# Kernel tuning notes

Measured on AMD Instinct MI355X. Metric: run time of the kernel, lower is better.

The kernel has to match this reference:

```python
import jax, jax.numpy as jnp
import numpy as np

LEVELS = 5          # perfect binary tree depth
N_NODES = 2**LEVELS - 1  # 31, level-order: children of p are 2p+1, 2p+2
V, E, ENC, H, LBL = 50000, 128, 128, 128, 104
B, L = 64, 128


def setup_inputs() -> dict:
    key = jax.random.key(0)
    ks = jax.random.split(key, 16)
    g = lambda k, shape: (jax.random.normal(k, shape, dtype=jnp.float32) * 0.02)
    return {
        "tokens": jax.random.randint(ks[0], (B, L, N_NODES), 0, V),
        "embedding": g(ks[1], (V, E)),
        "Wc_w": g(ks[2], (ENC, E)),
        "Wc_b": g(ks[3], (ENC,)),
        "Wih_f": g(ks[4], (3 * H, ENC)),
        "Whh_f": g(ks[5], (3 * H, H)),
        "bih_f": g(ks[6], (3 * H,)),
        "bhh_f": g(ks[7], (3 * H,)),
        "Wih_b": g(ks[8], (3 * H, ENC)),
        "Whh_b": g(ks[9], (3 * H, H)),
        "bih_b": g(ks[10], (3 * H,)),
        "bhh_b": g(ks[11], (3 * H,)),
        "Wout": g(ks[12], (LBL, 2 * H)),
        "bout": g(ks[13], (LBL,)),
    }


def _tree_encode(tokens, embedding, Wc_w, Wc_b):
    # node encoding h(n) = W_c(emb(tok_n)) + sum(children h); statement enc = max over nodes
    x = embedding[tokens]                       # [B, L, N, E] gather
    h = jnp.einsum("blne,ce->blnc", x, Wc_w) + Wc_b  # [B, L, N, ENC]
    for lvl in reversed(range(LEVELS - 1)):     # bottom-up accumulation
        s = 2**lvl - 1
        n = 2**lvl
        cs = 2 * s + 1                          # first child index of this level
        left = h[..., cs:cs + 2 * n:2, :]
        right = h[..., cs + 1:cs + 2 * n:2, :]
        h = h.at[..., s:s + n, :].add(left + right)
    # node_list max across all recursion calls == max over all tree nodes
    return jnp.max(h, axis=2)                   # [B, L, ENC]


def _gru_dir(xs, Wih, Whh, bih, bhh, reverse):
    # xs: [B, L, ENC]; PyTorch GRU cell equations, h0 = 0
    gi = jnp.einsum("blc,gc->blg", xs, Wih) + bih  # precompute input gates [B, L, 3H]
    h0 = jnp.zeros((xs.shape[0], H), dtype=xs.dtype)

    def step(h, gi_t):
        gh = h @ Whh.T + bhh
        ir, iz, inn = jnp.split(gi_t, 3, axis=-1)
        hr, hz, hn = jnp.split(gh, 3, axis=-1)
        r = jax.nn.sigmoid(ir + hr)
        z = jax.nn.sigmoid(iz + hz)
        n = jnp.tanh(inn + r * hn)
        h_new = (1.0 - z) * n + z * h
        return h_new, h_new

    _, ys = jax.lax.scan(step, h0, gi.transpose(1, 0, 2), reverse=reverse)
    return ys.transpose(1, 0, 2)                # [B, L, H]


def reference(tokens, embedding, Wc_w, Wc_b,
              Wih_f, Whh_f, bih_f, bhh_f,
              Wih_b, Whh_b, bih_b, bhh_b,
              Wout, bout):
    encodes = _tree_encode(tokens, embedding, Wc_w, Wc_b)   # [B, L, ENC]
    fwd = _gru_dir(encodes, Wih_f, Whh_f, bih_f, bhh_f, reverse=False)
    bwd = _gru_dir(encodes, Wih_b, Whh_b, bih_b, bhh_b, reverse=True)
    gru_out = jnp.concatenate([fwd, bwd], axis=-1)          # [B, L, 2H]
    pooled = jnp.max(gru_out, axis=1)                       # max_pool1d over time
    return pooled @ Wout.T + bout                           # [B, LBL]
```

## Files before the change

### kernel.cpp

```cpp
#include <hip/hip_runtime.h>
#include <hip/hip_bf16.h>
#include <math.h>

#define NN   31
#define VV   50000
#define EE   128
#define HH   128
#define BB   64
#define LL   128
#define NLBL 104

template <bool BIAS>
__global__ __launch_bounds__(256, 2) void gemm128(const float* __restrict__ A,
                                                  const float* __restrict__ B0,
                                                  const float* __restrict__ B1,
                                                  const float* __restrict__ bias0,
                                                  const float* __restrict__ bias1,
                                                  float* __restrict__ C0,
                                                  float* __restrict__ C1,
                                                  int M, int N) {
    const float* Bm  = blockIdx.z ? B1 : B0;
    const float* bias = blockIdx.z ? bias1 : bias0;
    float* C = blockIdx.z ? C1 : C0;

    __shared__ float4 As[64 * 17];
    __shared__ float4 Bs[128 * 17];
    const int tid = threadIdx.x;
    const int m0 = blockIdx.x * 64;
    const int n0 = blockIdx.y * 128;
    const float4* Af4 = (const float4*)A;
    const float4* Bf4 = (const float4*)Bm;

    const int r0 = (tid >> 4) * 4;
    const int cb = tid & 15;
    float acc[4][8] = {};

    for (int kk = 0; kk < 2; ++kk) {
        for (int f = tid; f < 128 * 16; f += 256) {
            int r = f >> 4, e = f & 15;
            Bs[r * 17 + e] = Bf4[(size_t)(n0 + r) * 32 + kk * 16 + e];
        }
        for (int f = tid; f < 64 * 16; f += 256) {
            int r = f >> 4, e = f & 15;
            float4 v = make_float4(0.f, 0.f, 0.f, 0.f);
            if (m0 + r < M) v = Af4[(size_t)(m0 + r) * 32 + kk * 16 + e];
            As[r * 17 + e] = v;
        }
        __syncthreads();
        #pragma unroll
        for (int e = 0; e < 16; ++e) {
            float4 a[4], b[8];
            #pragma unroll
            for (int i = 0; i < 4; ++i) a[i] = As[(r0 + i) * 17 + e];
            #pragma unroll
            for (int j = 0; j < 8; ++j) b[j] = Bs[(cb + j * 16) * 17 + e];
            #pragma unroll
            for (int i = 0; i < 4; ++i) {
                #pragma unroll
                for (int j = 0; j < 8; ++j) {
                    acc[i][j] += a[i].x * b[j].x;
                    acc[i][j] += a[i].y * b[j].y;
                    acc[i][j] += a[i].z * b[j].z;
                    acc[i][j] += a[i].w * b[j].w;
                }
            }
        }
        __syncthreads();
    }

    #pragma unroll
    for (int i = 0; i < 4; ++i) {
        int row = m0 + r0 + i;
        if (row < M) {
            #pragma unroll
            for (int j = 0; j < 8; ++j) {
                int col = n0 + cb + j * 16;
                float v = acc[i][j];
                if (BIAS) v += bias[col];
                C[(size_t)row * N + col] = v;
            }
        }
    }
}

__global__ __launch_bounds__(256) void tree_encode(const int* __restrict__ tok,
                                                   const float* __restrict__ Wemb,
                                                   const float* __restrict__ Wcb,
                                                   float* __restrict__ enc) {
    __shared__ int st[2][NN];
    const int tid = threadIdx.x;
    const int p = tid >> 7;
    const int c = tid & 127;
    const int bl = blockIdx.x * 2;
    if (tid < 2 * NN) {
        int pp = tid / NN, jj = tid - pp * NN;
        st[pp][jj] = tok[(size_t)(bl + pp) * NN + jj];
    }
    __syncthreads();

    float v[NN];
    #pragma unroll
    for (int j = 0; j < NN; ++j)
        v[j] = Wemb[(size_t)st[p][j] * 128 + c];
    #pragma unroll
    for (int i = 14; i >= 0; --i)
        v[i] += v[2 * i + 1] + v[2 * i + 2];

    const float wb = Wcb[c];
    float m = v[0] + 31.f * wb;
    #pragma unroll
    for (int i = 1; i <= 2; ++i)  m = fmaxf(m, v[i] + 15.f * wb);
    #pragma unroll
    for (int i = 3; i <= 6; ++i)  m = fmaxf(m, v[i] + 7.f * wb);
    #pragma unroll
    for (int i = 7; i <= 14; ++i) m = fmaxf(m, v[i] + 3.f * wb);
    #pragma unroll
    for (int i = 15; i <= 30; ++i) m = fmaxf(m, v[i] + wb);

    enc[(size_t)(bl + p) * 128 + c] = m;
}

__device__ __forceinline__ float sigm(float x) { return 1.f / (1.f + __expf(-x)); }
__device__ __forceinline__ float tanh_f(float x) { return 1.f - 2.f / (1.f + __expf(2.f * x)); }

__device__ __forceinline__ float dpp_xor1(float x) {
    return __builtin_bit_cast(float,
        __builtin_amdgcn_mov_dpp(__builtin_bit_cast(int, x), 0xB1, 0xF, 0xF, true));
}
__device__ __forceinline__ float dpp_xor2(float x) {
    return __builtin_bit_cast(float,
        __builtin_amdgcn_mov_dpp(__builtin_bit_cast(int, x), 0x4E, 0xF, 0xF, true));
}
__device__ __forceinline__ float quad_sum(float x) {
    x += dpp_xor1(x);
    x += dpp_xor2(x);
    return x;
}

__global__ __launch_bounds__(256, 1) void gru_scan(const float* __restrict__ gi_f,
                                                   const float* __restrict__ gi_b,
                                                   const float* __restrict__ Whh_f,
                                                   const float* __restrict__ Whh_b,
                                                   const float* __restrict__ bhh_f,
                                                   const float* __restrict__ bhh_b,
                                                   float* __restrict__ pooled) {
    const int tid = threadIdx.x;
    const int g   = tid >> 2;
    const int p   = tid & 3;
    const int dir = blockIdx.x & 1;
    const int b   = blockIdx.x >> 1;
    const float* gi  = dir ? gi_b  : gi_f;
    const float* Whh = dir ? Whh_b : Whh_f;
    const float* bhh = dir ? bhh_b : bhh_f;

    __shared__ __align__(16) float hbuf[2][128];

    float4 w[6][8];
    const float4* wf4 = (const float4*)Whh;
    #pragma unroll
    for (int r6 = 0; r6 < 6; ++r6)
        #pragma unroll
        for (int q = 0; q < 8; ++q)
            w[r6][q] = wf4[(size_t)(r6 * 64 + g) * 32 + p * 8 + q];

    const int c = g + p * 64;
    float bh_r = 0.f, bh_z = 0.f, bh_n = 0.f;
    if (p < 2) { bh_r = bhh[c]; bh_z = bhh[128 + c]; bh_n = bhh[256 + c]; }

    float hold = 0.f, m = -INFINITY;
    if (tid < 128) { hbuf[0][tid] = 0.f; }

    float gr = 0.f, gz = 0.f, gn = 0.f;
    {
        const int t0 = dir ? (LL - 1) : 0;
        const float* grow = gi + ((size_t)b * LL + t0) * 384;
        if (p < 2) { gr = grow[c]; gz = grow[128 + c]; gn = grow[256 + c]; }
    }
    __syncthreads();

    for (int s = 0; s < LL; ++s) {
        const int cur = s & 1;
        float gr_n = 0.f, gz_n = 0.f, gn_n = 0.f;
        if (p < 2 && s + 1 < LL) {
            const int t1 = dir ? (LL - 2 - s) : (s + 1);
            const float* grow = gi + ((size_t)b * LL + t1) * 384;
            gr_n = grow[c]; gz_n = grow[128 + c]; gn_n = grow[256 + c];
        }

        const float4* hq = ((const float4*)hbuf[cur]) + p * 8;
        float a0 = 0.f, a1 = 0.f, a2 = 0.f, a3 = 0.f, a4 = 0.f, a5 = 0.f;
        #pragma unroll
        for (int q = 0; q < 8; ++q) {
            const float4 hv = hq[q];
            a0 += w[0][q].x * hv.x + w[0][q].y * hv.y + w[0][q].z * hv.z + w[0][q].w * hv.w;
            a1 += w[1][q].x * hv.x + w[1][q].y * hv.y + w[1][q].z * hv.z + w[1][q].w * hv.w;
            a2 += w[2][q].x * hv.x + w[2][q].y * hv.y + w[2][q].z * hv.z + w[2][q].w * hv.w;
            a3 += w[3][q].x * hv.x + w[3][q].y * hv.y + w[3][q].z * hv.z + w[3][q].w * hv.w;
            a4 += w[4][q].x * hv.x + w[4][q].y * hv.y + w[4][q].z * hv.z + w[4][q].w * hv.w;
            a5 += w[5][q].x * hv.x + w[5][q].y * hv.y + w[5][q].z * hv.z + w[5][q].w * hv.w;
        }
        a0 = quad_sum(a0); a1 = quad_sum(a1); a2 = quad_sum(a2);
        a3 = quad_sum(a3); a4 = quad_sum(a4); a5 = quad_sum(a5);

        if (p < 2) {
            const float ghr = (p ? a1 : a0) + bh_r;
            const float ghz = (p ? a3 : a2) + bh_z;
            const float ghn = (p ? a5 : a4) + bh_n;
            const float r = sigm(gr + ghr);
            const float z = sigm(gz + ghz);
            const float n = tanh_f(gn + r * ghn);
            const float hn = (1.f - z) * n + z * hold;
            hold = hn;
            m = fmaxf(m, hn);
            hbuf[cur ^ 1][c] = hn;
        }
        gr = gr_n; gz = gz_n; gn = gn_n;
        __syncthreads();
    }
    if (p < 2) pooled[((size_t)b * 2 + dir) * 128 + c] = m;
}

__global__ __launch_bounds__(128) void out_head(const float* __restrict__ pooled,
                                                const float* __restrict__ Wout,
                                                const float* __restrict__ bout,
                                                float* __restrict__ out) {
    __shared__ __align__(16) float pbuf[256];
    const int b = blockIdx.x, o = threadIdx.x;
    if (o < 64) ((float4*)pbuf)[o] = ((const float4*)(pooled + (size_t)b * 256))[o];
    __syncthreads();
    if (o < NLBL) {
        float acc = bout[o];
        const float4* wf4 = (const float4*)(Wout + (size_t)o * 256);
        const float4* pf4 = (const float4*)pbuf;
        #pragma unroll 8
        for (int q = 0; q < 64; ++q) {
            float4 wv = wf4[q], pv = pf4[q];
            acc += wv.x * pv.x + wv.y * pv.y + wv.z * pv.z + wv.w * pv.w;
        }
        out[(size_t)b * NLBL + o] = acc;
    }
}

extern "C" void kernel_launch(void* const* d_in, const int* in_sizes, int n_in,
                              void* d_out, int out_size, void* d_ws, size_t ws_size,
                              hipStream_t stream) {
    const int*   tokens = (const int*)  d_in[0];
    const float* emb    = (const float*)d_in[1];
    const float* Wc_w   = (const float*)d_in[2];
    const float* Wc_b   = (const float*)d_in[3];
    const float* Wih_f  = (const float*)d_in[4];
    const float* Whh_f  = (const float*)d_in[5];
    const float* bih_f  = (const float*)d_in[6];
    const float* bhh_f  = (const float*)d_in[7];
    const float* Wih_b  = (const float*)d_in[8];
    const float* Whh_b  = (const float*)d_in[9];
    const float* bih_b  = (const float*)d_in[10];
    const float* bhh_b  = (const float*)d_in[11];
    const float* Wout   = (const float*)d_in[12];
    const float* bout   = (const float*)d_in[13];
    float* out = (float*)d_out;
    float* ws  = (float*)d_ws;

    float* Wemb = ws;
    float* enc  = Wemb + (size_t)VV * 128;
    float* gi_f = enc  + (size_t)BB * LL * 128;
    float* gi_b = gi_f + (size_t)BB * LL * 384;
    float* pool = gi_b + (size_t)BB * LL * 384;

    gemm128<false><<<dim3(782, 1, 1), 256, 0, stream>>>(
        emb, Wc_w, Wc_w, nullptr, nullptr, Wemb, Wemb, VV, 128);
    tree_encode<<<dim3(4096), 256, 0, stream>>>(tokens, Wemb, Wc_b, enc);
    gemm128<true><<<dim3(128, 3, 2), 256, 0, stream>>>(
        enc, Wih_f, Wih_b, bih_f, bih_b, gi_f, gi_b, BB * LL, 384);
    gru_scan<<<dim3(128), 256, 0, stream>>>(gi_f, gi_b, Whh_f, Whh_b, bhh_f, bhh_b, pool);
    out_head<<<dim3(64), 128, 0, stream>>>(pool, Wout, bout, out);
}
```

Before: 295.2 us.

## Widen GRU scan to 512 threads with one hidden unit per quad

The recurrent scan block grows from 256 to 512 threads. Each quad of four lanes now owns a single hidden unit's three gate rows, so every thread holds 24 float4 weights instead of 48 and the per-step dot-product chain is half as long. Shared-memory reads of h are rotated per lane to avoid bank conflicts, and the input-gate prefetch is deepened to two steps ahead. The cost is more waves per block synchronising at every timestep, and only one lane in four doing the gate math.

```diff
diff --git a/kernel.cpp b/kernel.cpp
--- a/kernel.cpp
+++ b/kernel.cpp
@@ -137,7 +137,7 @@
     return x;
 }
 
-__global__ __launch_bounds__(256, 1) void gru_scan(const float* __restrict__ gi_f,
+__global__ __launch_bounds__(512, 1) void gru_scan(const float* __restrict__ gi_f,
                                                    const float* __restrict__ gi_b,
                                                    const float* __restrict__ Whh_f,
                                                    const float* __restrict__ Whh_b,
@@ -145,7 +145,7 @@
                                                    const float* __restrict__ bhh_b,
                                                    float* __restrict__ pooled) {
     const int tid = threadIdx.x;
-    const int g   = tid >> 2;
+    const int c   = tid >> 2;
     const int p   = tid & 3;
     const int dir = blockIdx.x & 1;
     const int b   = blockIdx.x >> 1;
@@ -155,69 +155,63 @@
 
     __shared__ __align__(16) float hbuf[2][128];
 
-    float4 w[6][8];
+    float4 w[3][8];
     const float4* wf4 = (const float4*)Whh;
     #pragma unroll
-    for (int r6 = 0; r6 < 6; ++r6)
+    for (int r = 0; r < 3; ++r)
         #pragma unroll
-        for (int q = 0; q < 8; ++q)
-            w[r6][q] = wf4[(size_t)(r6 * 64 + g) * 32 + p * 8 + q];
-
-    const int c = g + p * 64;
+        for (int i = 0; i < 8; ++i)
+            w[r][i] = wf4[(size_t)(r * 128 + c) * 32 + p * 8 + ((i + 2 * p) & 7)];
+
     float bh_r = 0.f, bh_z = 0.f, bh_n = 0.f;
-    if (p < 2) { bh_r = bhh[c]; bh_z = bhh[128 + c]; bh_n = bhh[256 + c]; }
+    if (p == 0) { bh_r = bhh[c]; bh_z = bhh[128 + c]; bh_n = bhh[256 + c]; }
 
     float hold = 0.f, m = -INFINITY;
-    if (tid < 128) { hbuf[0][tid] = 0.f; }
-
-    float gr = 0.f, gz = 0.f, gn = 0.f;
-    {
-        const int t0 = dir ? (LL - 1) : 0;
-        const float* grow = gi + ((size_t)b * LL + t0) * 384;
-        if (p < 2) { gr = grow[c]; gz = grow[128 + c]; gn = grow[256 + c]; }
+    if (tid < 128) hbuf[0][tid] = 0.f;
+
+    float g0r = 0.f, g0z = 0.f, g0n = 0.f, g1r = 0.f, g1z = 0.f, g1n = 0.f;
+    if (p == 0) {
+        const float* row0 = gi + ((size_t)b * LL + (dir ? LL - 1 : 0)) * 384;
+        g0r = row0[c]; g0z = row0[128 + c]; g0n = row0[256 + c];
+        const float* row1 = gi + ((size_t)b * LL + (dir ? LL - 2 : 1)) * 384;
+        g1r = row1[c]; g1z = row1[128 + c]; g1n = row1[256 + c];
     }
     __syncthreads();
 
     for (int s = 0; s < LL; ++s) {
         const int cur = s & 1;
-        float gr_n = 0.f, gz_n = 0.f, gn_n = 0.f;
-        if (p < 2 && s + 1 < LL) {
-            const int t1 = dir ? (LL - 2 - s) : (s + 1);
-            const float* grow = gi + ((size_t)b * LL + t1) * 384;
-            gr_n = grow[c]; gz_n = grow[128 + c]; gn_n = grow[256 + c];
-        }
-
-        const float4* hq = ((const float4*)hbuf[cur]) + p * 8;
-        float a0 = 0.f, a1 = 0.f, a2 = 0.f, a3 = 0.f, a4 = 0.f, a5 = 0.f;
+        float g2r = 0.f, g2z = 0.f, g2n = 0.f;
+        if (p == 0 && s + 2 < LL) {
+            const int t2 = dir ? (LL - 3 - s) : (s + 2);
+            const float* row = gi + ((size_t)b * LL + t2) * 384;
+            g2r = row[c]; g2z = row[128 + c]; g2n = row[256 + c];
+        }
+
+        const float4* hq = (const float4*)hbuf[cur];
+        float a0 = 0.f, a1 = 0.f, a2 = 0.f;
         #pragma unroll
-        for (int q = 0; q < 8; ++q) {
-            const float4 hv = hq[q];
-            a0 += w[0][q].x * hv.x + w[0][q].y * hv.y + w[0][q].z * hv.z + w[0][q].w * hv.w;
-            a1 += w[1][q].x * hv.x + w[1][q].y * hv.y + w[1][q].z * hv.z + w[1][q].w * hv.w;
-            a2 += w[2][q].x * hv.x + w[2][q].y * hv.y + w[2][q].z * hv.z + w[2][q].w * hv.w;
-            a3 += w[3][q].x * hv.x + w[3][q].y * hv.y + w[3][q].z * hv.z + w[3][q].w * hv.w;
-            a4 += w[4][q].x * hv.x + w[4][q].y * hv.y + w[4][q].z * hv.z + w[4][q].w * hv.w;
-            a5 += w[5][q].x * hv.x + w[5][q].y * hv.y + w[5][q].z * hv.z + w[5][q].w * hv.w;
+        for (int i = 0; i < 8; ++i) {
+            const float4 hv = hq[p * 8 + ((i + 2 * p) & 7)];
+            a0 += w[0][i].x * hv.x + w[0][i].y * hv.y + w[0][i].z * hv.z + w[0][i].w * hv.w;
+            a1 += w[1][i].x * hv.x + w[1][i].y * hv.y + w[1][i].z * hv.z + w[1][i].w * hv.w;
+            a2 += w[2][i].x * hv.x + w[2][i].y * hv.y + w[2][i].z * hv.z + w[2][i].w * hv.w;
         }
         a0 = quad_sum(a0); a1 = quad_sum(a1); a2 = quad_sum(a2);
-        a3 = quad_sum(a3); a4 = quad_sum(a4); a5 = quad_sum(a5);
-
-        if (p < 2) {
-            const float ghr = (p ? a1 : a0) + bh_r;
-            const float ghz = (p ? a3 : a2) + bh_z;
-            const float ghn = (p ? a5 : a4) + bh_n;
-            const float r = sigm(gr + ghr);
-            const float z = sigm(gz + ghz);
-            const float n = tanh_f(gn + r * ghn);
+
+        if (p == 0) {
+            const float r = sigm(g0r + a0 + bh_r);
+            const float z = sigm(g0z + a1 + bh_z);
+            const float n = tanh_f(g0n + r * (a2 + bh_n));
             const float hn = (1.f - z) * n + z * hold;
             hold = hn;
             m = fmaxf(m, hn);
             hbuf[cur ^ 1][c] = hn;
         }
-        gr = gr_n; gz = gz_n; gn = gn_n;
+        g0r = g1r; g0z = g1z; g0n = g1n;
+        g1r = g2r; g1z = g2z; g1n = g2n;
         __syncthreads();
     }
-    if (p < 2) pooled[((size_t)b * 2 + dir) * 128 + c] = m;
+    if (p == 0) pooled[((size_t)b * 2 + dir) * 128 + c] = m;
 }
 
 __global__ __launch_bounds__(128) void out_head(const float* __restrict__ pooled,
@@ -272,6 +266,6 @@
     tree_encode<<<dim3(4096), 256, 0, stream>>>(tokens, Wemb, Wc_b, enc);
     gemm128<true><<<dim3(128, 3, 2), 256, 0, stream>>>(
         enc, Wih_f, Wih_b, bih_f, bih_b, gi_f, gi_b, BB * LL, 384);
-    gru_scan<<<dim3(128), 256, 0, stream>>>(gi_f, gi_b, Whh_f, Whh_b, bhh_f, bhh_b, pool);
+    gru_scan<<<dim3(128), 512, 0, stream>>>(gi_f, gi_b, Whh_f, Whh_b, bhh_f, bhh_b, pool);
     out_head<<<dim3(64), 128, 0, stream>>>(pool, Wout, bout, out);
 }
```

Result: faster. 284.2 us (-3.7%).
